# Kernel tuning notes

Measured on AMD Instinct MI355X. Metric: run time of the kernel, lower is better.

## Reference

```python
import jax, jax.numpy as jnp
import numpy as np

N_NODES = 200000
N_EDGES = 6400000
A_TOPO, A_PARAM, A_KCL, A_KVL, A_SPARSE = 1.0, 1.0, 0.1, 0.1, 0.01
EPS = 1e-6


def setup_inputs() -> dict:
    key = jax.random.key(0)
    k = jax.random.split(key, 7)
    # voltages near 1.0 p.u. (cols 0,1), loads small (cols 2,3)
    node_features = jnp.concatenate([
        1.0 + 0.05 * jax.random.normal(k[0], (N_NODES, 2), dtype=jnp.float32),
        0.1 * jax.random.normal(k[1], (N_NODES, 2), dtype=jnp.float32),
    ], axis=1)
    edge_index = jax.random.randint(k[2], (2, N_EDGES), 0, N_NODES)
    edge_logits = jax.random.normal(k[3], (N_EDGES,), dtype=jnp.float32)
    # R,X kept away from zero so 1/(R+eps) stays finite-scale
    edge_params = 0.1 + 0.5 * jax.random.uniform(k[4], (N_EDGES, 2), dtype=jnp.float32)
    edge_labels = (jax.random.uniform(k[5], (N_EDGES,)) < 0.5).astype(jnp.float32)
    target_edge_params = 0.1 + 0.5 * jax.random.uniform(k[6], (N_EDGES, 2), dtype=jnp.float32)
    return dict(node_features=node_features, edge_logits=edge_logits,
                edge_params=edge_params, edge_labels=edge_labels,
                target_edge_params=target_edge_params, edge_index=edge_index)


def _segsum(x, ids, n):
    return jax.ops.segment_sum(x, ids, num_segments=n)


def reference(node_features, edge_logits, edge_params, edge_labels,
              target_edge_params, edge_index):
    N = node_features.shape[0]
    src, dst = edge_index[0], edge_index[1]
    probs = jax.nn.sigmoid(edge_logits)                      # [E]
    R, X = edge_params[:, 0], edge_params[:, 1]

    # ---- topology: BCEWithLogits (mean) ----
    bce = -(edge_labels * jax.nn.log_sigmoid(edge_logits)
            + (1.0 - edge_labels) * jax.nn.log_sigmoid(-edge_logits))
    topology = A_TOPO * jnp.mean(bce)

    # ---- parameter: MSE ----
    parameter = A_PARAM * jnp.mean((edge_params - target_edge_params) ** 2)

    # ---- KCL: per-edge |I| = |v_src - v_dst| / |Z + 1e-6| (1e-6 added to real part) ----
    dvr = node_features[src, 0] - node_features[dst, 0]      # [E]
    dvi = node_features[src, 1] - node_features[dst, 1]
    cur = jnp.sqrt(dvr * dvr + dvi * dvi) / jnp.sqrt((R + EPS) ** 2 + X * X)
    curp = cur * probs
    # node sum: -|I|p at src, +|I|p at dst (self-loops cancel, same as original)
    node_cur = _segsum(curp, dst, N) - _segsum(curp, src, N)  # [N]
    kcl = A_KCL * jnp.mean(node_cur ** 2)

    # ---- KVL: parameter consistency + voltage-drop variance ----
    w = probs[:, None]                                       # [E,1]
    mean_params = (edge_params * w).sum(axis=0) / (probs.sum() + EPS)  # [2]
    param_var = (((edge_params - mean_params) ** 2) * w).sum(axis=0)   # [2]
    param_consistency = param_var.mean()
    vdrop = jnp.sqrt(dvr * dvr + dvi * dvi) * probs          # [E]
    voltage_consistency = jnp.var(vdrop, ddof=1)             # torch.var unbiased
    kvl = A_KVL * (param_consistency + voltage_consistency)

    # ---- radiality (weighted 0.1 in main loss) ----
    edge_count_loss = (probs.sum() - (N - 1)) ** 2
    radial = 0.1 * (1.0 * edge_count_loss + 0.1 * probs.mean())

    # ---- sparsity ----
    sparsity = A_SPARSE * probs.mean()

    return jnp.stack([topology, parameter, kcl, kvl, radial, sparsity,
                      topology + parameter + kcl + kvl + radial + sparsity])
```

## Files before the change

kernel.cpp:

```cpp
#include <hip/hip_runtime.h>


constexpr int   kNodes         = 200000;
constexpr int   kEdges         = 6400000;
constexpr int   kNumSums       = 9;
constexpr float kEps           = 1e-6f;

constexpr int   kBucketShift   = 12;
constexpr int   kBucketSize    = 1 << kBucketShift;
constexpr int   kBuckets       = (kNodes + kBucketSize - 1) / kBucketSize;
constexpr int   kEdgesPerBlk   = 1024;
constexpr int   kEdgesPerThr   = 4;
constexpr int   kP1Blocks      = kEdges / kEdgesPerBlk;
static_assert(kEdges % kEdgesPerBlk == 0, "exact tiling assumed");
constexpr int   kEntriesPerBlk = 2 * kEdgesPerBlk;
constexpr int   kOffStride     = 52;
constexpr int   kSlabs         = 16;
constexpr int   kTilesPerSlab  = (kP1Blocks + kSlabs - 1) / kSlabs;
constexpr int   kP2Blocks      = kBuckets * kSlabs;
constexpr int   kP2Threads     = 512;
constexpr int   kP2Waves       = kP2Threads / 64;
constexpr int   kNodeBlocks    = 200;
constexpr int   kFbBlocks      = 2048;
constexpr float kQScale        = 65536.0f;
constexpr float kQInv          = 1.0f / 65536.0f;
constexpr int   kQBias         = 524288;

__device__ __forceinline__ float softplusf(float t) {
    return fmaxf(t, 0.0f) + log1pf(expf(-fabsf(t)));
}

__global__ __launch_bounds__(256) void compact_nf(
    const float4* __restrict__ nf4,
    float2*       __restrict__ nfc)
{
    const int i = blockIdx.x * 256 + threadIdx.x;
    if (i < kNodes) {
        const float4 v = nf4[i];
        nfc[i] = make_float2(v.x, v.y);
    }
}

__global__ __launch_bounds__(256) void p1_edges(
    const float2* __restrict__ nfc,
    const float*  __restrict__ logits,
    const float*  __restrict__ eparams,
    const float*  __restrict__ labels,
    const float*  __restrict__ tparams,
    const int*    __restrict__ srcs,
    const int*    __restrict__ dsts,
    unsigned*       __restrict__ pairs,
    unsigned short* __restrict__ offs_g,
    float*          __restrict__ partials)
{
    __shared__ __align__(16) unsigned sorted[kEntriesPerBlk];
    __shared__ int   hist[kBuckets];
    __shared__ int   offs[kBuckets + 1];
    __shared__ float smem[4][kNumSums];

    const int tid = threadIdx.x;
    if (tid < kBuckets) hist[tid] = 0;
    __syncthreads();

    float acc[kNumSums];
#pragma unroll
    for (int k = 0; k < kNumSums; ++k) acc[k] = 0.0f;

    unsigned ent[2 * kEdgesPerThr];
    int      rnk[2 * kEdgesPerThr];
    int      bkt[2 * kEdgesPerThr];

    const int e0 = blockIdx.x * kEdgesPerBlk;
    const int q4 = (e0 >> 2) + tid;

    const int4 ss = reinterpret_cast<const int4*>(srcs)[q4];
    const int4 dd = reinterpret_cast<const int4*>(dsts)[q4];

    const float2 vs0 = nfc[ss.x];
    const float2 vs1 = nfc[ss.y];
    const float2 vs2 = nfc[ss.z];
    const float2 vs3 = nfc[ss.w];
    const float2 vd0 = nfc[dd.x];
    const float2 vd1 = nfc[dd.y];
    const float2 vd2 = nfc[dd.z];
    const float2 vd3 = nfc[dd.w];

    const float4 lx = reinterpret_cast<const float4*>(logits)[q4];
    const float4 ly = reinterpret_cast<const float4*>(labels)[q4];
    const float4 ea = reinterpret_cast<const float4*>(eparams)[2 * q4];
    const float4 eb = reinterpret_cast<const float4*>(eparams)[2 * q4 + 1];
    const float4 ta = reinterpret_cast<const float4*>(tparams)[2 * q4];
    const float4 tb = reinterpret_cast<const float4*>(tparams)[2 * q4 + 1];

    const float xs[4]  = {lx.x, lx.y, lx.z, lx.w};
    const float ys[4]  = {ly.x, ly.y, ly.z, ly.w};
    const float epr[4] = {ea.x, ea.z, eb.x, eb.z};
    const float epx[4] = {ea.y, ea.w, eb.y, eb.w};
    const float tpr[4] = {ta.x, ta.z, tb.x, tb.z};
    const float tpx[4] = {ta.y, ta.w, tb.y, tb.w};
    const float2 vss[4] = {vs0, vs1, vs2, vs3};
    const float2 vdd[4] = {vd0, vd1, vd2, vd3};
    const int    sn[4]  = {ss.x, ss.y, ss.z, ss.w};
    const int    dn[4]  = {dd.x, dd.y, dd.z, dd.w};

#pragma unroll
    for (int j = 0; j < kEdgesPerThr; ++j) {
        const float x = xs[j], y = ys[j];
        const float er = epr[j], ex = epx[j];

        const float t      = __expf(-fabsf(x));
        const float inv1pt = __builtin_amdgcn_rcpf(1.0f + t);
        const float p      = (x >= 0.0f) ? inv1pt : t * inv1pt;
        const float sp_nx  = fmaxf(-x, 0.0f) + __logf(1.0f + t);
        const float bce    = sp_nx + (1.0f - y) * x;

        const float dr  = er - tpr[j];
        const float dxx = ex - tpx[j];

        const float dvr = vss[j].x - vdd[j].x;
        const float dvi = vss[j].y - vdd[j].y;
        const float mag = sqrtf(dvr * dvr + dvi * dvi);

        const float Rp    = er + kEps;
        const float curp  = mag * rsqrtf(Rp * Rp + ex * ex) * p;
        const float vdrop = mag * p;

        acc[0] += bce;
        acc[1] += dr * dr + dxx * dxx;
        acc[2] += p;
        acc[3] += p * er;
        acc[4] += p * ex;
        acc[5] += p * er * er;
        acc[6] += p * ex * ex;
        acc[7] += vdrop;
        acc[8] += vdrop * vdrop;

        int q = __float2int_rn(curp * kQScale);
        q = max(-(kQBias - 1), min(kQBias - 1, q));

        const int bd = dn[j] >> kBucketShift;
        const int bs = sn[j] >> kBucketShift;
        rnk[2 * j]     = atomicAdd(&hist[bd], 1);
        rnk[2 * j + 1] = atomicAdd(&hist[bs], 1);
        bkt[2 * j]     = bd;
        bkt[2 * j + 1] = bs;

        ent[2 * j]     = ((unsigned)(dn[j] & (kBucketSize - 1)) << 20) | (unsigned)( q + kQBias);
        ent[2 * j + 1] = ((unsigned)(sn[j] & (kBucketSize - 1)) << 20) | (unsigned)(-q + kQBias);
    }

    __syncthreads();

    {
        const int lane = tid & 63;
        int h    = (lane < kBuckets) ? hist[lane] : 0;
        int incl = h;
#pragma unroll
        for (int o = 1; o < 64; o <<= 1) {
            int n = __shfl_up(incl, o, 64);
            if (lane >= o) incl += n;
        }
        if (lane < kBuckets + 1) offs[lane] = incl - h;
    }

#pragma unroll
    for (int k = 0; k < 2 * kEdgesPerThr; ++k)
        sorted[offs[bkt[k]] + rnk[k]] = ent[k];

    __syncthreads();

    {
        const uint4 v0 = *reinterpret_cast<const uint4*>(&sorted[tid * 4]);
        reinterpret_cast<uint4*>(pairs + (size_t)blockIdx.x * kEntriesPerBlk)[tid] = v0;
        const uint4 v1 = *reinterpret_cast<const uint4*>(&sorted[1024 + tid * 4]);
        reinterpret_cast<uint4*>(pairs + (size_t)blockIdx.x * kEntriesPerBlk)[256 + tid] = v1;
    }
    if (tid < kBuckets + 1)
        offs_g[(size_t)blockIdx.x * kOffStride + tid] = (unsigned short)offs[tid];

    const int lane = tid & 63;
    const int wave = tid >> 6;
#pragma unroll
    for (int k = 0; k < kNumSums; ++k) {
        float v = acc[k];
#pragma unroll
        for (int off = 32; off > 0; off >>= 1) v += __shfl_down(v, off, 64);
        if (lane == 0) smem[wave][k] = v;
    }
    __syncthreads();
    if (tid < kNumSums) {
        float v = 0.0f;
#pragma unroll
        for (int w = 0; w < 4; ++w) v += smem[w][tid];
        partials[blockIdx.x * kNumSums + tid] = v;
    }
}

__global__ __launch_bounds__(kP2Threads) void p2_buckets(
    const unsigned*       __restrict__ pairs,
    const unsigned short* __restrict__ offs_g,
    int*                  __restrict__ out_i32)
{
    __shared__ int accs[kBucketSize];
    const int b    = blockIdx.x / kSlabs;
    const int slab = blockIdx.x % kSlabs;

    for (int i = threadIdx.x; i < kBucketSize; i += kP2Threads) accs[i] = 0;
    __syncthreads();

    const int i0 = slab * kTilesPerSlab;
    const int i1 = min(i0 + kTilesPerSlab, kP1Blocks);
    const int lane = threadIdx.x & 63;
    const int wave = threadIdx.x >> 6;

    int i = i0 + wave;
    if (i < i1) {
        int o0 = (int)offs_g[(size_t)i * kOffStride + b];
        int o1 = (int)offs_g[(size_t)i * kOffStride + b + 1];
        unsigned u    = 0;
        bool     has  = (o0 + lane) < o1;
        if (has) u = pairs[(size_t)i * kEntriesPerBlk + o0 + lane];

        for (; i < i1; ) {
            const int ni = i + kP2Waves;
            int no0 = 0, no1 = 0;
            unsigned nu = 0;
            bool nhas = false;
            if (ni < i1) {
                no0 = (int)offs_g[(size_t)ni * kOffStride + b];
                no1 = (int)offs_g[(size_t)ni * kOffStride + b + 1];
                nhas = (no0 + lane) < no1;
                if (nhas) nu = pairs[(size_t)ni * kEntriesPerBlk + no0 + lane];
            }

            if (has) atomicAdd(&accs[u >> 20], (int)(u & 0xFFFFFu) - kQBias);
            const unsigned* pb = pairs + (size_t)i * kEntriesPerBlk;
            for (int j = o0 + 64 + lane; j < o1; j += 64) {
                const unsigned w = pb[j];
                atomicAdd(&accs[w >> 20], (int)(w & 0xFFFFFu) - kQBias);
            }

            i = ni; o0 = no0; o1 = no1; u = nu; has = nhas;
        }
    }
    __syncthreads();

    int* o = out_i32 + (size_t)blockIdx.x * kBucketSize;
    for (int i2 = threadIdx.x; i2 < kBucketSize; i2 += kP2Threads) o[i2] = accs[i2];
}

__global__ __launch_bounds__(256) void node_pass_binned(
    const int* __restrict__ out_i32,
    float*     __restrict__ node_partials)
{
    float acc = 0.0f;
    const int stride = gridDim.x * blockDim.x;
    for (int n4 = blockIdx.x * blockDim.x + threadIdx.x; n4 < kNodes / 4; n4 += stride) {
        const int n = n4 * 4;
        const int b = n >> kBucketShift;
        const int s = n & (kBucketSize - 1);
        const int* p = out_i32 + ((size_t)b * kSlabs) * kBucketSize + s;
        int4 v = make_int4(0, 0, 0, 0);
#pragma unroll
        for (int m = 0; m < kSlabs; ++m) {
            const int4 w = *reinterpret_cast<const int4*>(p + (size_t)m * kBucketSize);
            v.x += w.x; v.y += w.y; v.z += w.z; v.w += w.w;
        }
        const float f0 = (float)v.x * kQInv;
        const float f1 = (float)v.y * kQInv;
        const float f2 = (float)v.z * kQInv;
        const float f3 = (float)v.w * kQInv;
        acc += f0 * f0 + f1 * f1 + f2 * f2 + f3 * f3;
    }
    __shared__ float smem[4];
    const int lane = threadIdx.x & 63;
    const int wave = threadIdx.x >> 6;
    float v = acc;
#pragma unroll
    for (int off = 32; off > 0; off >>= 1) v += __shfl_down(v, off, 64);
    if (lane == 0) smem[wave] = v;
    __syncthreads();
    if (threadIdx.x == 0)
        node_partials[blockIdx.x] = smem[0] + smem[1] + smem[2] + smem[3];
}

__global__ __launch_bounds__(256) void edge_pass_atomic(
    const float* __restrict__ nf, const float* __restrict__ logits,
    const float* __restrict__ eparams, const float* __restrict__ labels,
    const float* __restrict__ tparams, const int* __restrict__ srcs,
    const int* __restrict__ dsts, float* __restrict__ node_cur,
    float* __restrict__ partials)
{
    float acc[kNumSums];
#pragma unroll
    for (int k = 0; k < kNumSums; ++k) acc[k] = 0.0f;
    const int stride = gridDim.x * blockDim.x;
    for (int e = blockIdx.x * blockDim.x + threadIdx.x; e < kEdges; e += stride) {
        float  x  = logits[e];
        float  y  = labels[e];
        float2 ep = *reinterpret_cast<const float2*>(eparams + 2 * e);
        float2 tp = *reinterpret_cast<const float2*>(tparams + 2 * e);
        int    s  = srcs[e];
        int    d  = dsts[e];
        float2 vs = *reinterpret_cast<const float2*>(nf + 4 * s);
        float2 vd = *reinterpret_cast<const float2*>(nf + 4 * d);
        float p   = 1.0f / (1.0f + expf(-x));
        float bce = y * softplusf(-x) + (1.0f - y) * softplusf(x);
        float dr = ep.x - tp.x, dxx = ep.y - tp.y;
        float dvr = vs.x - vd.x, dvi = vs.y - vd.y;
        float mag = sqrtf(dvr * dvr + dvi * dvi);
        float Rp  = ep.x + kEps;
        float den = sqrtf(Rp * Rp + ep.y * ep.y);
        float curp = (mag / den) * p;
        float vdrop = mag * p;
        acc[0] += bce; acc[1] += dr * dr + dxx * dxx; acc[2] += p;
        acc[3] += p * ep.x; acc[4] += p * ep.y;
        acc[5] += p * ep.x * ep.x; acc[6] += p * ep.y * ep.y;
        acc[7] += vdrop; acc[8] += vdrop * vdrop;
        atomicAdd(node_cur + d,  curp);
        atomicAdd(node_cur + s, -curp);
    }
    __shared__ float smem[4][kNumSums];
    const int lane = threadIdx.x & 63, wave = threadIdx.x >> 6;
#pragma unroll
    for (int k = 0; k < kNumSums; ++k) {
        float v = acc[k];
#pragma unroll
        for (int off = 32; off > 0; off >>= 1) v += __shfl_down(v, off, 64);
        if (lane == 0) smem[wave][k] = v;
    }
    __syncthreads();
    if (threadIdx.x < kNumSums) {
        float v = 0.0f;
#pragma unroll
        for (int w = 0; w < 4; ++w) v += smem[w][threadIdx.x];
        partials[blockIdx.x * kNumSums + threadIdx.x] = v;
    }
}

__global__ __launch_bounds__(256) void node_pass_flat(
    const float* __restrict__ node_cur, float* __restrict__ node_partials)
{
    float acc = 0.0f;
    const int stride = gridDim.x * blockDim.x;
    for (int i = blockIdx.x * blockDim.x + threadIdx.x; i < kNodes; i += stride) {
        float v = node_cur[i];
        acc += v * v;
    }
    __shared__ float smem[4];
    const int lane = threadIdx.x & 63, wave = threadIdx.x >> 6;
    float v = acc;
#pragma unroll
    for (int off = 32; off > 0; off >>= 1) v += __shfl_down(v, off, 64);
    if (lane == 0) smem[wave] = v;
    __syncthreads();
    if (threadIdx.x == 0)
        node_partials[blockIdx.x] = smem[0] + smem[1] + smem[2] + smem[3];
}

__global__ __launch_bounds__(256) void finalize(
    const float* __restrict__ partials, int nblocks,
    const float* __restrict__ node_partials, int nnp,
    float*       __restrict__ out)
{
    const int tid  = threadIdx.x;
    const int lane = tid & 63;
    const int wave = tid >> 6;
    __shared__ double red[4][kNumSums + 1];

    double s[kNumSums];
#pragma unroll
    for (int k = 0; k < kNumSums; ++k) s[k] = 0.0;
    for (int i = tid; i < nblocks; i += 256) {
#pragma unroll
        for (int k = 0; k < kNumSums; ++k)
            s[k] += (double)partials[i * kNumSums + k];
    }
    double ns = 0.0;
    for (int i = tid; i < nnp; i += 256) ns += (double)node_partials[i];

#pragma unroll
    for (int k = 0; k < kNumSums + 1; ++k) {
        double v = (k < kNumSums) ? s[k] : ns;
#pragma unroll
        for (int off = 32; off > 0; off >>= 1) v += __shfl_down(v, off, 64);
        if (lane == 0) red[wave][k] = v;
    }
    __syncthreads();

    if (tid == 0) {
        double sums[kNumSums + 1];
#pragma unroll
        for (int k = 0; k < kNumSums + 1; ++k)
            sums[k] = red[0][k] + red[1][k] + red[2][k] + red[3][k];

        const double E = (double)kEdges, N = (double)kNodes;
        const double s_bce = sums[0], s_par = sums[1], s_p = sums[2];
        const double s_pR = sums[3], s_pX = sums[4];
        const double s_pR2 = sums[5], s_pX2 = sums[6];
        const double s_v = sums[7], s_v2 = sums[8];
        const double nsum = sums[9];

        double topology  = s_bce / E;
        double parameter = s_par / (2.0 * E);
        double kcl       = 0.1 * (nsum / N);

        double denom = s_p + (double)kEps;
        double mR = s_pR / denom, mX = s_pX / denom;
        double varR = s_pR2 - 2.0 * mR * s_pR + mR * mR * s_p;
        double varX = s_pX2 - 2.0 * mX * s_pX + mX * mX * s_p;
        double param_consistency = 0.5 * (varR + varX);
        double voltage_consistency = (s_v2 - (s_v * s_v) / E) / (E - 1.0);
        double kvl = 0.1 * (param_consistency + voltage_consistency);

        double ecl = s_p - (N - 1.0);
        ecl = ecl * ecl;
        double radial   = 0.1 * (ecl + 0.1 * (s_p / E));
        double sparsity = 0.01 * (s_p / E);
        double total = topology + parameter + kcl + kvl + radial + sparsity;

        out[0] = (float)topology;  out[1] = (float)parameter;
        out[2] = (float)kcl;       out[3] = (float)kvl;
        out[4] = (float)radial;    out[5] = (float)sparsity;
        out[6] = (float)total;
    }
}

extern "C" void kernel_launch(void* const* d_in, const int* in_sizes, int n_in,
                              void* d_out, int out_size, void* d_ws, size_t ws_size,
                              hipStream_t stream) {
    const float* nf      = (const float*)d_in[0];
    const float* logits  = (const float*)d_in[1];
    const float* eparams = (const float*)d_in[2];
    const float* labels  = (const float*)d_in[3];
    const float* tparams = (const float*)d_in[4];
    const int*   eidx    = (const int*)d_in[5];
    float* out           = (float*)d_out;

    const size_t n_pairs  = (size_t)kP1Blocks * kEntriesPerBlk;
    const size_t n_outi32 = (size_t)kP2Blocks * kBucketSize;
    const size_t n_nfc    = (size_t)kNodes * 2;
    const size_t n_offs_w = ((size_t)kP1Blocks * kOffStride + 1) / 2 + 64;
    const size_t n_words  = n_pairs + n_outi32 + n_nfc + n_offs_w +
                            (size_t)kP1Blocks * kNumSums + kNodeBlocks;

    if (ws_size >= n_words * sizeof(unsigned)) {
        unsigned*       pairs         = (unsigned*)d_ws;
        int*            out_i32       = (int*)(pairs + n_pairs);
        float2*         nfc           = (float2*)(out_i32 + n_outi32);
        unsigned short* offs_g        = (unsigned short*)((unsigned*)nfc + n_nfc);
        float*          partials      = (float*)((unsigned*)offs_g + n_offs_w);
        float*          node_partials = partials + (size_t)kP1Blocks * kNumSums;

        compact_nf<<<(kNodes + 255) / 256, 256, 0, stream>>>(
            (const float4*)nf, nfc);
        p1_edges<<<kP1Blocks, 256, 0, stream>>>(nfc, logits, eparams, labels,
                                                tparams, eidx, eidx + kEdges,
                                                pairs, offs_g, partials);
        p2_buckets<<<kP2Blocks, kP2Threads, 0, stream>>>(pairs, offs_g, out_i32);
        node_pass_binned<<<kNodeBlocks, 256, 0, stream>>>(out_i32, node_partials);
        finalize<<<1, 256, 0, stream>>>(partials, kP1Blocks, node_partials,
                                        kNodeBlocks, out);
    } else {
        float* node_cur      = (float*)d_ws;
        float* partials      = node_cur + kNodes;
        float* node_partials = partials + (size_t)kFbBlocks * kNumSums;

        hipMemsetAsync(node_cur, 0, kNodes * sizeof(float), stream);
        edge_pass_atomic<<<kFbBlocks, 256, 0, stream>>>(nf, logits, eparams, labels,
                                                        tparams, eidx, eidx + kEdges,
                                                        node_cur, partials);
        node_pass_flat<<<kNodeBlocks, 256, 0, stream>>>(node_cur, node_partials);
        finalize<<<1, 256, 0, stream>>>(partials, kFbBlocks, node_partials,
                                        kNodeBlocks, out);
    }
}
```

Measured before the change: 139.8 us.

## Process two edge tiles per block in p1, overlapping tile B loads with tile A sort

Each p1 block now handles two 1024-edge tiles with separate LDS histograms and sort buffers. The index, gather and edge-data loads for the second tile are issued during the first tile's scan, LDS scatter and global write, so memory latency overlaps with LDS work. Full __syncthreads are replaced by a barrier that waits only on LDS counters, leaving global loads in flight across it. This halves the block count and raises register and LDS use per block, which may reduce occupancy.

```diff
diff --git a/kernel.cpp b/kernel.cpp
--- a/kernel.cpp
+++ b/kernel.cpp
@@ -9,14 +9,14 @@
 constexpr int   kBucketShift   = 12;
 constexpr int   kBucketSize    = 1 << kBucketShift;
 constexpr int   kBuckets       = (kNodes + kBucketSize - 1) / kBucketSize;
-constexpr int   kEdgesPerBlk   = 1024;
-constexpr int   kEdgesPerThr   = 4;
-constexpr int   kP1Blocks      = kEdges / kEdgesPerBlk;
-static_assert(kEdges % kEdgesPerBlk == 0, "exact tiling assumed");
-constexpr int   kEntriesPerBlk = 2 * kEdgesPerBlk;
+constexpr int   kTileEdges     = 1024;
+constexpr int   kTiles         = kEdges / kTileEdges;
+constexpr int   kP1Blocks      = kTiles / 2;
+static_assert(kEdges % (2 * kTileEdges) == 0, "exact tiling assumed");
+constexpr int   kTileEnt       = 2 * kTileEdges;
 constexpr int   kOffStride     = 52;
 constexpr int   kSlabs         = 16;
-constexpr int   kTilesPerSlab  = (kP1Blocks + kSlabs - 1) / kSlabs;
+constexpr int   kTilesPerSlab  = (kTiles + kSlabs - 1) / kSlabs;
 constexpr int   kP2Blocks      = kBuckets * kSlabs;
 constexpr int   kP2Threads     = 512;
 constexpr int   kP2Waves       = kP2Threads / 64;
@@ -28,6 +28,12 @@
 
 __device__ __forceinline__ float softplusf(float t) {
     return fmaxf(t, 0.0f) + log1pf(expf(-fabsf(t)));
+}
+
+__device__ __forceinline__ void wg_barrier_lds() {
+    asm volatile("s_waitcnt lgkmcnt(0)" ::: "memory");
+    __builtin_amdgcn_s_barrier();
+    asm volatile("" ::: "memory");
 }
 
 __global__ __launch_bounds__(256) void compact_nf(
@@ -53,130 +59,236 @@
     unsigned short* __restrict__ offs_g,
     float*          __restrict__ partials)
 {
-    __shared__ __align__(16) unsigned sorted[kEntriesPerBlk];
-    __shared__ int   hist[kBuckets];
-    __shared__ int   offs[kBuckets + 1];
+    __shared__ __align__(16) unsigned sortedA[kTileEnt];
+    __shared__ __align__(16) unsigned sortedB[kTileEnt];
+    __shared__ int   histA[kBuckets], histB[kBuckets];
+    __shared__ int   offsA[kBuckets + 1], offsB[kBuckets + 1];
     __shared__ float smem[4][kNumSums];
 
     const int tid = threadIdx.x;
-    if (tid < kBuckets) hist[tid] = 0;
+    if (tid < kBuckets) { histA[tid] = 0; histB[tid] = 0; }
     __syncthreads();
 
     float acc[kNumSums];
 #pragma unroll
     for (int k = 0; k < kNumSums; ++k) acc[k] = 0.0f;
 
-    unsigned ent[2 * kEdgesPerThr];
-    int      rnk[2 * kEdgesPerThr];
-    int      bkt[2 * kEdgesPerThr];
-
-    const int e0 = blockIdx.x * kEdgesPerBlk;
-    const int q4 = (e0 >> 2) + tid;
-
-    const int4 ss = reinterpret_cast<const int4*>(srcs)[q4];
-    const int4 dd = reinterpret_cast<const int4*>(dsts)[q4];
-
-    const float2 vs0 = nfc[ss.x];
-    const float2 vs1 = nfc[ss.y];
-    const float2 vs2 = nfc[ss.z];
-    const float2 vs3 = nfc[ss.w];
-    const float2 vd0 = nfc[dd.x];
-    const float2 vd1 = nfc[dd.y];
-    const float2 vd2 = nfc[dd.z];
-    const float2 vd3 = nfc[dd.w];
-
-    const float4 lx = reinterpret_cast<const float4*>(logits)[q4];
-    const float4 ly = reinterpret_cast<const float4*>(labels)[q4];
-    const float4 ea = reinterpret_cast<const float4*>(eparams)[2 * q4];
-    const float4 eb = reinterpret_cast<const float4*>(eparams)[2 * q4 + 1];
-    const float4 ta = reinterpret_cast<const float4*>(tparams)[2 * q4];
-    const float4 tb = reinterpret_cast<const float4*>(tparams)[2 * q4 + 1];
-
-    const float xs[4]  = {lx.x, lx.y, lx.z, lx.w};
-    const float ys[4]  = {ly.x, ly.y, ly.z, ly.w};
-    const float epr[4] = {ea.x, ea.z, eb.x, eb.z};
-    const float epx[4] = {ea.y, ea.w, eb.y, eb.w};
-    const float tpr[4] = {ta.x, ta.z, tb.x, tb.z};
-    const float tpx[4] = {ta.y, ta.w, tb.y, tb.w};
-    const float2 vss[4] = {vs0, vs1, vs2, vs3};
-    const float2 vdd[4] = {vd0, vd1, vd2, vd3};
-    const int    sn[4]  = {ss.x, ss.y, ss.z, ss.w};
-    const int    dn[4]  = {dd.x, dd.y, dd.z, dd.w};
-
-#pragma unroll
-    for (int j = 0; j < kEdgesPerThr; ++j) {
-        const float x = xs[j], y = ys[j];
-        const float er = epr[j], ex = epx[j];
-
-        const float t      = __expf(-fabsf(x));
-        const float inv1pt = __builtin_amdgcn_rcpf(1.0f + t);
-        const float p      = (x >= 0.0f) ? inv1pt : t * inv1pt;
-        const float sp_nx  = fmaxf(-x, 0.0f) + __logf(1.0f + t);
-        const float bce    = sp_nx + (1.0f - y) * x;
-
-        const float dr  = er - tpr[j];
-        const float dxx = ex - tpx[j];
-
-        const float dvr = vss[j].x - vdd[j].x;
-        const float dvi = vss[j].y - vdd[j].y;
-        const float mag = sqrtf(dvr * dvr + dvi * dvi);
-
-        const float Rp    = er + kEps;
-        const float curp  = mag * rsqrtf(Rp * Rp + ex * ex) * p;
-        const float vdrop = mag * p;
-
-        acc[0] += bce;
-        acc[1] += dr * dr + dxx * dxx;
-        acc[2] += p;
-        acc[3] += p * er;
-        acc[4] += p * ex;
-        acc[5] += p * er * er;
-        acc[6] += p * ex * ex;
-        acc[7] += vdrop;
-        acc[8] += vdrop * vdrop;
-
-        int q = __float2int_rn(curp * kQScale);
-        q = max(-(kQBias - 1), min(kQBias - 1, q));
-
-        const int bd = dn[j] >> kBucketShift;
-        const int bs = sn[j] >> kBucketShift;
-        rnk[2 * j]     = atomicAdd(&hist[bd], 1);
-        rnk[2 * j + 1] = atomicAdd(&hist[bs], 1);
-        bkt[2 * j]     = bd;
-        bkt[2 * j + 1] = bs;
-
-        ent[2 * j]     = ((unsigned)(dn[j] & (kBucketSize - 1)) << 20) | (unsigned)( q + kQBias);
-        ent[2 * j + 1] = ((unsigned)(sn[j] & (kBucketSize - 1)) << 20) | (unsigned)(-q + kQBias);
-    }
-
-    __syncthreads();
+    const int tA = 2 * blockIdx.x;
+    const int tB = tA + 1;
+    const int qA = tA * 256 + tid;
+    const int qB = tB * 256 + tid;
+
+    const int4 ssA = reinterpret_cast<const int4*>(srcs)[qA];
+    const int4 ddA = reinterpret_cast<const int4*>(dsts)[qA];
+
+    const float2 avs0 = nfc[ssA.x];
+    const float2 avs1 = nfc[ssA.y];
+    const float2 avs2 = nfc[ssA.z];
+    const float2 avs3 = nfc[ssA.w];
+    const float2 avd0 = nfc[ddA.x];
+    const float2 avd1 = nfc[ddA.y];
+    const float2 avd2 = nfc[ddA.z];
+    const float2 avd3 = nfc[ddA.w];
+
+    const float4 alx = reinterpret_cast<const float4*>(logits)[qA];
+    const float4 aly = reinterpret_cast<const float4*>(labels)[qA];
+    const float4 aea = reinterpret_cast<const float4*>(eparams)[2 * qA];
+    const float4 aeb = reinterpret_cast<const float4*>(eparams)[2 * qA + 1];
+    const float4 ata = reinterpret_cast<const float4*>(tparams)[2 * qA];
+    const float4 atb = reinterpret_cast<const float4*>(tparams)[2 * qA + 1];
+
+    const int4 ssB = reinterpret_cast<const int4*>(srcs)[qB];
+    const int4 ddB = reinterpret_cast<const int4*>(dsts)[qB];
+
+    unsigned entA[8];
+    int      rnkA[8], bktA[8];
+
+    {
+        const float xs[4]  = {alx.x, alx.y, alx.z, alx.w};
+        const float ys[4]  = {aly.x, aly.y, aly.z, aly.w};
+        const float epr[4] = {aea.x, aea.z, aeb.x, aeb.z};
+        const float epx[4] = {aea.y, aea.w, aeb.y, aeb.w};
+        const float tpr[4] = {ata.x, ata.z, atb.x, atb.z};
+        const float tpx[4] = {ata.y, ata.w, atb.y, atb.w};
+        const float2 vss[4] = {avs0, avs1, avs2, avs3};
+        const float2 vdd[4] = {avd0, avd1, avd2, avd3};
+        const int    sn[4]  = {ssA.x, ssA.y, ssA.z, ssA.w};
+        const int    dn[4]  = {ddA.x, ddA.y, ddA.z, ddA.w};
+
+#pragma unroll
+        for (int j = 0; j < 4; ++j) {
+            const float x = xs[j], y = ys[j];
+            const float er = epr[j], ex = epx[j];
+
+            const float t      = __expf(-fabsf(x));
+            const float inv1pt = __builtin_amdgcn_rcpf(1.0f + t);
+            const float p      = (x >= 0.0f) ? inv1pt : t * inv1pt;
+            const float sp_nx  = fmaxf(-x, 0.0f) + __logf(1.0f + t);
+            const float bce    = sp_nx + (1.0f - y) * x;
+
+            const float dr  = er - tpr[j];
+            const float dxx = ex - tpx[j];
+            const float dvr = vss[j].x - vdd[j].x;
+            const float dvi = vss[j].y - vdd[j].y;
+            const float mag = sqrtf(dvr * dvr + dvi * dvi);
+            const float Rp    = er + kEps;
+            const float curp  = mag * rsqrtf(Rp * Rp + ex * ex) * p;
+            const float vdrop = mag * p;
+
+            acc[0] += bce;
+            acc[1] += dr * dr + dxx * dxx;
+            acc[2] += p;
+            acc[3] += p * er;
+            acc[4] += p * ex;
+            acc[5] += p * er * er;
+            acc[6] += p * ex * ex;
+            acc[7] += vdrop;
+            acc[8] += vdrop * vdrop;
+
+            int q = __float2int_rn(curp * kQScale);
+            q = max(-(kQBias - 1), min(kQBias - 1, q));
+
+            const int bd = dn[j] >> kBucketShift;
+            const int bs = sn[j] >> kBucketShift;
+            rnkA[2 * j]     = atomicAdd(&histA[bd], 1);
+            rnkA[2 * j + 1] = atomicAdd(&histA[bs], 1);
+            bktA[2 * j]     = bd;
+            bktA[2 * j + 1] = bs;
+            entA[2 * j]     = ((unsigned)(dn[j] & (kBucketSize - 1)) << 20) | (unsigned)( q + kQBias);
+            entA[2 * j + 1] = ((unsigned)(sn[j] & (kBucketSize - 1)) << 20) | (unsigned)(-q + kQBias);
+        }
+    }
+
+    wg_barrier_lds();
+
+    const float2 bvs0 = nfc[ssB.x];
+    const float2 bvs1 = nfc[ssB.y];
+    const float2 bvs2 = nfc[ssB.z];
+    const float2 bvs3 = nfc[ssB.w];
+    const float2 bvd0 = nfc[ddB.x];
+    const float2 bvd1 = nfc[ddB.y];
+    const float2 bvd2 = nfc[ddB.z];
+    const float2 bvd3 = nfc[ddB.w];
+
+    const float4 blx = reinterpret_cast<const float4*>(logits)[qB];
+    const float4 bly = reinterpret_cast<const float4*>(labels)[qB];
+    const float4 bea = reinterpret_cast<const float4*>(eparams)[2 * qB];
+    const float4 beb = reinterpret_cast<const float4*>(eparams)[2 * qB + 1];
+    const float4 bta = reinterpret_cast<const float4*>(tparams)[2 * qB];
+    const float4 btb = reinterpret_cast<const float4*>(tparams)[2 * qB + 1];
 
     {
         const int lane = tid & 63;
-        int h    = (lane < kBuckets) ? hist[lane] : 0;
+        int h    = (lane < kBuckets) ? histA[lane] : 0;
         int incl = h;
 #pragma unroll
         for (int o = 1; o < 64; o <<= 1) {
             int n = __shfl_up(incl, o, 64);
             if (lane >= o) incl += n;
         }
-        if (lane < kBuckets + 1) offs[lane] = incl - h;
-    }
-
-#pragma unroll
-    for (int k = 0; k < 2 * kEdgesPerThr; ++k)
-        sorted[offs[bkt[k]] + rnk[k]] = ent[k];
-
-    __syncthreads();
+        if (lane < kBuckets + 1) offsA[lane] = incl - h;
+    }
+
+#pragma unroll
+    for (int k = 0; k < 8; ++k)
+        sortedA[offsA[bktA[k]] + rnkA[k]] = entA[k];
+
+    wg_barrier_lds();
 
     {
-        const uint4 v0 = *reinterpret_cast<const uint4*>(&sorted[tid * 4]);
-        reinterpret_cast<uint4*>(pairs + (size_t)blockIdx.x * kEntriesPerBlk)[tid] = v0;
-        const uint4 v1 = *reinterpret_cast<const uint4*>(&sorted[1024 + tid * 4]);
-        reinterpret_cast<uint4*>(pairs + (size_t)blockIdx.x * kEntriesPerBlk)[256 + tid] = v1;
+        const uint4 v0 = *reinterpret_cast<const uint4*>(&sortedA[tid * 4]);
+        reinterpret_cast<uint4*>(pairs + (size_t)tA * kTileEnt)[tid] = v0;
+        const uint4 v1 = *reinterpret_cast<const uint4*>(&sortedA[1024 + tid * 4]);
+        reinterpret_cast<uint4*>(pairs + (size_t)tA * kTileEnt)[256 + tid] = v1;
     }
     if (tid < kBuckets + 1)
-        offs_g[(size_t)blockIdx.x * kOffStride + tid] = (unsigned short)offs[tid];
+        offs_g[(size_t)tA * kOffStride + tid] = (unsigned short)offsA[tid];
+
+    unsigned entB[8];
+    int      rnkB[8], bktB[8];
+    {
+        const float xs[4]  = {blx.x, blx.y, blx.z, blx.w};
+        const float ys[4]  = {bly.x, bly.y, bly.z, bly.w};
+        const float epr[4] = {bea.x, bea.z, beb.x, beb.z};
+        const float epx[4] = {bea.y, bea.w, beb.y, beb.w};
+        const float tpr[4] = {bta.x, bta.z, btb.x, btb.z};
+        const float tpx[4] = {bta.y, bta.w, btb.y, btb.w};
+        const float2 vss[4] = {bvs0, bvs1, bvs2, bvs3};
+        const float2 vdd[4] = {bvd0, bvd1, bvd2, bvd3};
+        const int    sn[4]  = {ssB.x, ssB.y, ssB.z, ssB.w};
+        const int    dn[4]  = {ddB.x, ddB.y, ddB.z, ddB.w};
+
+#pragma unroll
+        for (int j = 0; j < 4; ++j) {
+            const float x = xs[j], y = ys[j];
+            const float er = epr[j], ex = epx[j];
+
+            const float t      = __expf(-fabsf(x));
+            const float inv1pt = __builtin_amdgcn_rcpf(1.0f + t);
+            const float p      = (x >= 0.0f) ? inv1pt : t * inv1pt;
+            const float sp_nx  = fmaxf(-x, 0.0f) + __logf(1.0f + t);
+            const float bce    = sp_nx + (1.0f - y) * x;
+
+            const float dr  = er - tpr[j];
+            const float dxx = ex - tpx[j];
+            const float dvr = vss[j].x - vdd[j].x;
+            const float dvi = vss[j].y - vdd[j].y;
+            const float mag = sqrtf(dvr * dvr + dvi * dvi);
+            const float Rp    = er + kEps;
+            const float curp  = mag * rsqrtf(Rp * Rp + ex * ex) * p;
+            const float vdrop = mag * p;
+
+            acc[0] += bce;
+            acc[1] += dr * dr + dxx * dxx;
+            acc[2] += p;
+            acc[3] += p * er;
+            acc[4] += p * ex;
+            acc[5] += p * er * er;
+            acc[6] += p * ex * ex;
+            acc[7] += vdrop;
+            acc[8] += vdrop * vdrop;
+
+            int q = __float2int_rn(curp * kQScale);
+            q = max(-(kQBias - 1), min(kQBias - 1, q));
+
+            const int bd = dn[j] >> kBucketShift;
+            const int bs = sn[j] >> kBucketShift;
+            rnkB[2 * j]     = atomicAdd(&histB[bd], 1);
+            rnkB[2 * j + 1] = atomicAdd(&histB[bs], 1);
+            bktB[2 * j]     = bd;
+            bktB[2 * j + 1] = bs;
+            entB[2 * j]     = ((unsigned)(dn[j] & (kBucketSize - 1)) << 20) | (unsigned)( q + kQBias);
+            entB[2 * j + 1] = ((unsigned)(sn[j] & (kBucketSize - 1)) << 20) | (unsigned)(-q + kQBias);
+        }
+    }
+
+    wg_barrier_lds();
+
+    {
+        const int lane = tid & 63;
+        int h    = (lane < kBuckets) ? histB[lane] : 0;
+        int incl = h;
+#pragma unroll
+        for (int o = 1; o < 64; o <<= 1) {
+            int n = __shfl_up(incl, o, 64);
+            if (lane >= o) incl += n;
+        }
+        if (lane < kBuckets + 1) offsB[lane] = incl - h;
+    }
+#pragma unroll
+    for (int k = 0; k < 8; ++k)
+        sortedB[offsB[bktB[k]] + rnkB[k]] = entB[k];
+
+    wg_barrier_lds();
+
+    {
+        const uint4 v0 = *reinterpret_cast<const uint4*>(&sortedB[tid * 4]);
+        reinterpret_cast<uint4*>(pairs + (size_t)tB * kTileEnt)[tid] = v0;
+        const uint4 v1 = *reinterpret_cast<const uint4*>(&sortedB[1024 + tid * 4]);
+        reinterpret_cast<uint4*>(pairs + (size_t)tB * kTileEnt)[256 + tid] = v1;
+    }
+    if (tid < kBuckets + 1)
+        offs_g[(size_t)tB * kOffStride + tid] = (unsigned short)offsB[tid];
 
     const int lane = tid & 63;
     const int wave = tid >> 6;
@@ -209,7 +321,7 @@
     __syncthreads();
 
     const int i0 = slab * kTilesPerSlab;
-    const int i1 = min(i0 + kTilesPerSlab, kP1Blocks);
+    const int i1 = min(i0 + kTilesPerSlab, kTiles);
     const int lane = threadIdx.x & 63;
     const int wave = threadIdx.x >> 6;
 
@@ -219,7 +331,7 @@
         int o1 = (int)offs_g[(size_t)i * kOffStride + b + 1];
         unsigned u    = 0;
         bool     has  = (o0 + lane) < o1;
-        if (has) u = pairs[(size_t)i * kEntriesPerBlk + o0 + lane];
+        if (has) u = pairs[(size_t)i * kTileEnt + o0 + lane];
 
         for (; i < i1; ) {
             const int ni = i + kP2Waves;
@@ -230,11 +342,11 @@
                 no0 = (int)offs_g[(size_t)ni * kOffStride + b];
                 no1 = (int)offs_g[(size_t)ni * kOffStride + b + 1];
                 nhas = (no0 + lane) < no1;
-                if (nhas) nu = pairs[(size_t)ni * kEntriesPerBlk + no0 + lane];
+                if (nhas) nu = pairs[(size_t)ni * kTileEnt + no0 + lane];
             }
 
             if (has) atomicAdd(&accs[u >> 20], (int)(u & 0xFFFFFu) - kQBias);
-            const unsigned* pb = pairs + (size_t)i * kEntriesPerBlk;
+            const unsigned* pb = pairs + (size_t)i * kTileEnt;
             for (int j = o0 + 64 + lane; j < o1; j += 64) {
                 const unsigned w = pb[j];
                 atomicAdd(&accs[w >> 20], (int)(w & 0xFFFFFu) - kQBias);
@@ -437,12 +549,12 @@
     const int*   eidx    = (const int*)d_in[5];
     float* out           = (float*)d_out;
 
-    const size_t n_pairs  = (size_t)kP1Blocks * kEntriesPerBlk;
+    const size_t n_pairs  = (size_t)kTiles * kTileEnt;
     const size_t n_outi32 = (size_t)kP2Blocks * kBucketSize;
     const size_t n_nfc    = (size_t)kNodes * 2;
-    const size_t n_offs_w = ((size_t)kP1Blocks * kOffStride + 1) / 2 + 64;
+    const size_t n_offs_w = ((size_t)kTiles * kOffStride + 1) / 2 + 64;
     const size_t n_words  = n_pairs + n_outi32 + n_nfc + n_offs_w +
-                            (size_t)kP1Blocks * kNumSums + kNodeBlocks;
+                            (size_t)kTiles * kNumSums + kNodeBlocks;
 
     if (ws_size >= n_words * sizeof(unsigned)) {
         unsigned*       pairs         = (unsigned*)d_ws;
@@ -450,7 +562,7 @@
         float2*         nfc           = (float2*)(out_i32 + n_outi32);
         unsigned short* offs_g        = (unsigned short*)((unsigned*)nfc + n_nfc);
         float*          partials      = (float*)((unsigned*)offs_g + n_offs_w);
-        float*          node_partials = partials + (size_t)kP1Blocks * kNumSums;
+        float*          node_partials = partials + (size_t)kTiles * kNumSums;
 
         compact_nf<<<(kNodes + 255) / 256, 256, 0, stream>>>(
             (const float4*)nf, nfc);
```

Result: faster. 136.6 us (-2.3%).
